# Kernel optimization log

Measured on AMD Instinct MI355X. Metric: run time of the kernel, lower is better.

Reference implementation:

```python
import jax, jax.numpy as jnp
import numpy as np

# FP4 (E2M1) code table: nibble = [sign(1) | exp(2) | mantissa(1)]
# magnitudes for codes 0..7: 0, 0.5, 1, 1.5, 2, 3, 4, 6; codes 8..15 are negated.
_MAG = np.array([0.0, 0.5, 1.0, 1.5, 2.0, 3.0, 4.0, 6.0], dtype=np.float32)
FP4_LUT = jnp.asarray(np.concatenate([_MAG, -_MAG]))  # [16]

BLOCK = 16  # scale-factor block size along in_features


def setup_inputs() -> dict:
    key = jax.random.key(0)
    k0, k1, k2, k3, k4 = jax.random.split(key, 5)
    M, K, N = 32, 8192, 8192  # tokens, in_features, out_features
    inp = jax.random.normal(k0, (M, K), dtype=jnp.float32)
    qweight = jax.random.randint(k1, (N, K // 2), 0, 256, dtype=jnp.int32)  # packed FP4 pairs
    scales = jax.random.uniform(k2, (N, K // BLOCK), dtype=jnp.float32)      # per-block scales
    amax = jax.random.uniform(k3, (1,), dtype=jnp.float32) + 0.5             # global scale
    bias = jax.random.normal(k4, (N,), dtype=jnp.float32)
    return {"input": inp, "qweight": qweight, "scales": scales, "amax": amax, "bias": bias}


def _dequantize(qweight, scales, amax):
    N = qweight.shape[0]
    low = qweight & 0xF            # first element of each pair
    high = (qweight >> 4) & 0xF    # second element
    nibbles = jnp.stack([low, high], axis=-1).reshape(N, -1)  # [N, K]
    vals = FP4_LUT[nibbles]                                   # [N, K] fp4 values
    # per-block scaling: block of BLOCK contiguous in-features shares one scale
    w = (vals.reshape(N, -1, BLOCK) * scales[..., None]).reshape(N, -1)
    return w * amax[0]


def reference(input, qweight, scales, amax, bias):
    weight = _dequantize(qweight, scales, amax)   # [N, K] full-precision weight
    return input @ weight.T + bias                # F.linear
```

## Files before the change

kernel.cpp:

```cpp
#include <hip/hip_runtime.h>
#include <hip/hip_bf16.h>

#define M_DIM 32
#define K_DIM 8192
#define N_DIM 8192
#define KS 8
#define KCH (K_DIM / KS)
#define NGROUPS (N_DIM / 32)
#define TOTAL_WAVES (NGROUPS * KS)
#define MAIN_BLOCKS (TOTAL_WAVES / 4)

typedef _Float16 half8 __attribute__((ext_vector_type(8)));
typedef float floatx4 __attribute__((ext_vector_type(4)));

__device__ __forceinline__ uint32_t dec2(uint32_t q) {
  uint32_t c0 = q & 0xFu, c1 = (q >> 4) & 0xFu;
  uint32_t m0 = c0 & 7u, m1 = c1 & 7u;
  uint32_t t0 = (m0 >= 2u) ? (m0 + 28u) : (m0 ? 28u : 0u);
  uint32_t t1 = (m1 >= 2u) ? (m1 + 28u) : (m1 ? 28u : 0u);
  return (t0 << 9) | ((c0 & 8u) << 12)
       | (t1 << 25) | ((c1 & 8u) << 28);
}

__device__ __forceinline__ half8 decode8(int4 q, float scale) {
  union { uint32_t u[4]; half8 h; } w;
  w.u[0] = dec2((uint32_t)q.x);
  w.u[1] = dec2((uint32_t)q.y);
  w.u[2] = dec2((uint32_t)q.z);
  w.u[3] = dec2((uint32_t)q.w);
  _Float16 s = (_Float16)scale;
  half8 sv = {s, s, s, s, s, s, s, s};
  return w.h * sv;
}

__device__ __forceinline__ half8 loadA(const float* __restrict__ inp, int m, int kq) {
  const floatx4* p = reinterpret_cast<const floatx4*>(inp + m * K_DIM + kq);
  floatx4 f0 = p[0];
  floatx4 f1 = p[1];
  half8 a;
  a[0] = (_Float16)f0[0]; a[1] = (_Float16)f0[1];
  a[2] = (_Float16)f0[2]; a[3] = (_Float16)f0[3];
  a[4] = (_Float16)f1[0]; a[5] = (_Float16)f1[1];
  a[6] = (_Float16)f1[2]; a[7] = (_Float16)f1[3];
  return a;
}

__global__ void init_out_kernel(float* __restrict__ out, const float* __restrict__ bias) {
  int idx = blockIdx.x * blockDim.x + threadIdx.x;
  if (idx < M_DIM * N_DIM) out[idx] = bias[idx & (N_DIM - 1)];
}

__global__ __launch_bounds__(256, 2) void fp4_linear_kernel(
    const float* __restrict__ inp,
    const int4*  __restrict__ qw4,
    const float* __restrict__ scales,
    const float* __restrict__ amaxp,
    float* __restrict__ out)
{
  const int lane = threadIdx.x & 63;
  const int wave = blockIdx.x * 4 + (threadIdx.x >> 6);
  const int ng   = wave & (NGROUPS - 1);
  const int ks   = wave >> 8;
  const int n0   = ng * 32;
  const int kb   = ks * KCH;

  const int row  = lane & 15;
  const int quad = lane >> 4;

  const float amax = amaxp[0];

  floatx4 acc00 = {0.f, 0.f, 0.f, 0.f};
  floatx4 acc01 = {0.f, 0.f, 0.f, 0.f};
  floatx4 acc10 = {0.f, 0.f, 0.f, 0.f};
  floatx4 acc11 = {0.f, 0.f, 0.f, 0.f};

  const int nA = n0 + row;
  const int nB = n0 + 16 + row;
  const int4*  qrowA = qw4 + (size_t)nA * (K_DIM / 8);
  const int4*  qrowB = qw4 + (size_t)nB * (K_DIM / 8);
  const float* srowA = scales + (size_t)nA * (K_DIM / 16);
  const float* srowB = scales + (size_t)nB * (K_DIM / 16);

  for (int k0 = kb; k0 < kb + KCH; k0 += 32) {
    const int kq = k0 + quad * 8;
    int4  qA = qrowA[kq >> 3];
    int4  qB = qrowB[kq >> 3];
    float sA = srowA[kq >> 4] * amax;
    float sB = srowB[kq >> 4] * amax;
    half8 bA = decode8(qA, sA);
    half8 bB = decode8(qB, sB);
    half8 a0 = loadA(inp, row, kq);
    half8 a1 = loadA(inp, row + 16, kq);

    acc00 = __builtin_amdgcn_mfma_f32_16x16x32_f16(a0, bA, acc00, 0, 0, 0);
    acc01 = __builtin_amdgcn_mfma_f32_16x16x32_f16(a0, bB, acc01, 0, 0, 0);
    acc10 = __builtin_amdgcn_mfma_f32_16x16x32_f16(a1, bA, acc10, 0, 0, 0);
    acc11 = __builtin_amdgcn_mfma_f32_16x16x32_f16(a1, bB, acc11, 0, 0, 0);
  }

#pragma unroll
  for (int r = 0; r < 4; ++r) {
    const int m = quad * 4 + r;
    unsafeAtomicAdd(&out[(size_t)m * N_DIM + n0 + row],            acc00[r]);
    unsafeAtomicAdd(&out[(size_t)m * N_DIM + n0 + 16 + row],       acc01[r]);
    unsafeAtomicAdd(&out[(size_t)(m + 16) * N_DIM + n0 + row],      acc10[r]);
    unsafeAtomicAdd(&out[(size_t)(m + 16) * N_DIM + n0 + 16 + row], acc11[r]);
  }
}

extern "C" void kernel_launch(void* const* d_in, const int* in_sizes, int n_in,
                              void* d_out, int out_size, void* d_ws, size_t ws_size,
                              hipStream_t stream) {
  const float* inp    = (const float*)d_in[0];
  const int4*  qw4    = (const int4*)d_in[1];
  const float* scales = (const float*)d_in[2];
  const float* amaxp  = (const float*)d_in[3];
  const float* bias   = (const float*)d_in[4];
  float* out = (float*)d_out;

  init_out_kernel<<<(M_DIM * N_DIM + 255) / 256, 256, 0, stream>>>(out, bias);
  fp4_linear_kernel<<<MAIN_BLOCKS, 256, 0, stream>>>(inp, qw4, scales, amaxp, out);
}
```

Before: 262.2 us.

## Prefetch loads, use hardware FP4 convert, pre-convert input, LDS-reduce split-K partials

Several ideas land together. The K split doubles to 16, and the four waves of a block now work on the same N group so their partial sums are added in shared memory before one atomic per output. Loads are software-pipelined one iteration ahead, and FP4 decode uses the gfx950 scaled convert builtin when it is available. The fp32 input is converted once to fp16 in the workspace, and the bias init is vectorised. These target load latency, decode ALU work, redundant activation conversion and atomic traffic, at the cost of an extra kernel launch and more shared memory per block.

```diff
diff --git a/kernel.cpp b/kernel.cpp
--- a/kernel.cpp
+++ b/kernel.cpp
@@ -4,63 +4,99 @@
 #define M_DIM 32
 #define K_DIM 8192
 #define N_DIM 8192
-#define KS 8
+#define KS 16
 #define KCH (K_DIM / KS)
+#define ITERS (KCH / 32)
 #define NGROUPS (N_DIM / 32)
-#define TOTAL_WAVES (NGROUPS * KS)
-#define MAIN_BLOCKS (TOTAL_WAVES / 4)
+#define MAIN_BLOCKS (NGROUPS * KS / 4)
 
-typedef _Float16 half8 __attribute__((ext_vector_type(8)));
-typedef float floatx4 __attribute__((ext_vector_type(4)));
+typedef _Float16 half8   __attribute__((ext_vector_type(8)));
+typedef _Float16 half4_t __attribute__((ext_vector_type(4)));
+typedef _Float16 half2_t __attribute__((ext_vector_type(2)));
+typedef float    floatx4 __attribute__((ext_vector_type(4)));
 
+#if defined(__has_builtin)
+#if __has_builtin(__builtin_amdgcn_cvt_scalef32_pk_f16_fp4)
+#define HAVE_CVT_FP4 1
+#endif
+#endif
+
+#ifndef HAVE_CVT_FP4
 __device__ __forceinline__ uint32_t dec2(uint32_t q) {
   uint32_t c0 = q & 0xFu, c1 = (q >> 4) & 0xFu;
   uint32_t m0 = c0 & 7u, m1 = c1 & 7u;
-  uint32_t t0 = (m0 >= 2u) ? (m0 + 28u) : (m0 ? 28u : 0u);
-  uint32_t t1 = (m1 >= 2u) ? (m1 + 28u) : (m1 ? 28u : 0u);
+  uint32_t t0 = min(28u * m0, m0 + 28u);
+  uint32_t t1 = min(28u * m1, m1 + 28u);
   return (t0 << 9) | ((c0 & 8u) << 12)
        | (t1 << 25) | ((c1 & 8u) << 28);
 }
+#endif
 
 __device__ __forceinline__ half8 decode8(int4 q, float scale) {
-  union { uint32_t u[4]; half8 h; } w;
+  union { uint32_t u[4]; half2_t h2[4]; half8 h; } w;
+#ifdef HAVE_CVT_FP4
+  w.h2[0] = __builtin_amdgcn_cvt_scalef32_pk_f16_fp4((unsigned)q.x, 1.0f, 0);
+  w.h2[1] = __builtin_amdgcn_cvt_scalef32_pk_f16_fp4((unsigned)q.y, 1.0f, 0);
+  w.h2[2] = __builtin_amdgcn_cvt_scalef32_pk_f16_fp4((unsigned)q.z, 1.0f, 0);
+  w.h2[3] = __builtin_amdgcn_cvt_scalef32_pk_f16_fp4((unsigned)q.w, 1.0f, 0);
+#else
   w.u[0] = dec2((uint32_t)q.x);
   w.u[1] = dec2((uint32_t)q.y);
   w.u[2] = dec2((uint32_t)q.z);
   w.u[3] = dec2((uint32_t)q.w);
+#endif
   _Float16 s = (_Float16)scale;
   half8 sv = {s, s, s, s, s, s, s, s};
   return w.h * sv;
 }
 
-__device__ __forceinline__ half8 loadA(const float* __restrict__ inp, int m, int kq) {
-  const floatx4* p = reinterpret_cast<const floatx4*>(inp + m * K_DIM + kq);
-  floatx4 f0 = p[0];
-  floatx4 f1 = p[1];
-  half8 a;
-  a[0] = (_Float16)f0[0]; a[1] = (_Float16)f0[1];
-  a[2] = (_Float16)f0[2]; a[3] = (_Float16)f0[3];
-  a[4] = (_Float16)f1[0]; a[5] = (_Float16)f1[1];
-  a[6] = (_Float16)f1[2]; a[7] = (_Float16)f1[3];
-  return a;
+template <bool F16A>
+__device__ __forceinline__ half8 loadA(const void* __restrict__ A, int m, int kq) {
+  if constexpr (F16A) {
+    return *reinterpret_cast<const half8*>(
+        (const _Float16*)A + (size_t)m * K_DIM + kq);
+  } else {
+    const floatx4* p =
+        reinterpret_cast<const floatx4*>((const float*)A + (size_t)m * K_DIM + kq);
+    floatx4 f0 = p[0];
+    floatx4 f1 = p[1];
+    half8 a;
+    a[0] = (_Float16)f0[0]; a[1] = (_Float16)f0[1];
+    a[2] = (_Float16)f0[2]; a[3] = (_Float16)f0[3];
+    a[4] = (_Float16)f1[0]; a[5] = (_Float16)f1[1];
+    a[6] = (_Float16)f1[2]; a[7] = (_Float16)f1[3];
+    return a;
+  }
 }
 
-__global__ void init_out_kernel(float* __restrict__ out, const float* __restrict__ bias) {
+__global__ void init_out_kernel(floatx4* __restrict__ out4,
+                                const floatx4* __restrict__ bias4) {
   int idx = blockIdx.x * blockDim.x + threadIdx.x;
-  if (idx < M_DIM * N_DIM) out[idx] = bias[idx & (N_DIM - 1)];
+  out4[idx] = bias4[idx & (N_DIM / 4 - 1)];
 }
 
-__global__ __launch_bounds__(256, 2) void fp4_linear_kernel(
-    const float* __restrict__ inp,
-    const int4*  __restrict__ qw4,
+__global__ void convertA_kernel(const floatx4* __restrict__ in4,
+                                half4_t* __restrict__ out4) {
+  int idx = blockIdx.x * blockDim.x + threadIdx.x;
+  floatx4 f = in4[idx];
+  half4_t h;
+  h[0] = (_Float16)f[0]; h[1] = (_Float16)f[1];
+  h[2] = (_Float16)f[2]; h[3] = (_Float16)f[3];
+  out4[idx] = h;
+}
+
+template <bool F16A>
+__global__ __launch_bounds__(256, 4) void fp4_linear_kernel(
+    const void* __restrict__ Av,
+    const int4* __restrict__ qw4,
     const float* __restrict__ scales,
     const float* __restrict__ amaxp,
     float* __restrict__ out)
 {
   const int lane = threadIdx.x & 63;
-  const int wave = blockIdx.x * 4 + (threadIdx.x >> 6);
-  const int ng   = wave & (NGROUPS - 1);
-  const int ks   = wave >> 8;
+  const int w    = threadIdx.x >> 6;
+  const int ng   = blockIdx.x >> 2;
+  const int ks   = (blockIdx.x & 3) * 4 + w;
   const int n0   = ng * 32;
   const int kb   = ks * KCH;
 
@@ -81,30 +117,56 @@
   const float* srowA = scales + (size_t)nA * (K_DIM / 16);
   const float* srowB = scales + (size_t)nB * (K_DIM / 16);
 
-  for (int k0 = kb; k0 < kb + KCH; k0 += 32) {
-    const int kq = k0 + quad * 8;
-    int4  qA = qrowA[kq >> 3];
-    int4  qB = qrowB[kq >> 3];
-    float sA = srowA[kq >> 4] * amax;
-    float sB = srowB[kq >> 4] * amax;
-    half8 bA = decode8(qA, sA);
-    half8 bB = decode8(qB, sB);
-    half8 a0 = loadA(inp, row, kq);
-    half8 a1 = loadA(inp, row + 16, kq);
+  int kq = kb + quad * 8;
+  int4  qA = qrowA[kq >> 3];
+  int4  qB = qrowB[kq >> 3];
+  float sA = srowA[kq >> 4];
+  float sB = srowB[kq >> 4];
+  half8 a0 = loadA<F16A>(Av, row, kq);
+  half8 a1 = loadA<F16A>(Av, row + 16, kq);
 
+#pragma unroll 4
+  for (int it = 0; it < ITERS; ++it) {
+    const int kqn  = kq + 32;
+    const int qidx = min(kqn >> 3, K_DIM / 8 - 1);
+    const int sidx = min(kqn >> 4, K_DIM / 16 - 1);
+    const int aidx = min(kqn, K_DIM - 8);
+    int4  qA_n = qrowA[qidx];
+    int4  qB_n = qrowB[qidx];
+    float sA_n = srowA[sidx];
+    float sB_n = srowB[sidx];
+    half8 a0_n = loadA<F16A>(Av, row, aidx);
+    half8 a1_n = loadA<F16A>(Av, row + 16, aidx);
+
+    half8 bA = decode8(qA, sA * amax);
+    half8 bB = decode8(qB, sB * amax);
     acc00 = __builtin_amdgcn_mfma_f32_16x16x32_f16(a0, bA, acc00, 0, 0, 0);
     acc01 = __builtin_amdgcn_mfma_f32_16x16x32_f16(a0, bB, acc01, 0, 0, 0);
     acc10 = __builtin_amdgcn_mfma_f32_16x16x32_f16(a1, bA, acc10, 0, 0, 0);
     acc11 = __builtin_amdgcn_mfma_f32_16x16x32_f16(a1, bB, acc11, 0, 0, 0);
+
+    qA = qA_n; qB = qB_n; sA = sA_n; sB = sB_n; a0 = a0_n; a1 = a1_n;
+    kq = kqn;
   }
 
+  __shared__ float red[4 * 32 * 34];
+  float* slab = red + w * (32 * 34);
 #pragma unroll
   for (int r = 0; r < 4; ++r) {
     const int m = quad * 4 + r;
-    unsafeAtomicAdd(&out[(size_t)m * N_DIM + n0 + row],            acc00[r]);
-    unsafeAtomicAdd(&out[(size_t)m * N_DIM + n0 + 16 + row],       acc01[r]);
-    unsafeAtomicAdd(&out[(size_t)(m + 16) * N_DIM + n0 + row],      acc10[r]);
-    unsafeAtomicAdd(&out[(size_t)(m + 16) * N_DIM + n0 + 16 + row], acc11[r]);
+    slab[m * 34 + row]             = acc00[r];
+    slab[m * 34 + 16 + row]        = acc01[r];
+    slab[(m + 16) * 34 + row]      = acc10[r];
+    slab[(m + 16) * 34 + 16 + row] = acc11[r];
+  }
+  __syncthreads();
+#pragma unroll
+  for (int i = 0; i < 4; ++i) {
+    const int o = i * 256 + threadIdx.x;
+    const int m = o >> 5, n = o & 31;
+    const int a = m * 34 + n;
+    float v = red[a] + red[1088 + a] + red[2 * 1088 + a] + red[3 * 1088 + a];
+    unsafeAtomicAdd(&out[(size_t)m * N_DIM + n0 + n], v);
   }
 }
 
@@ -118,6 +180,17 @@
   const float* bias   = (const float*)d_in[4];
   float* out = (float*)d_out;
 
-  init_out_kernel<<<(M_DIM * N_DIM + 255) / 256, 256, 0, stream>>>(out, bias);
-  fp4_linear_kernel<<<MAIN_BLOCKS, 256, 0, stream>>>(inp, qw4, scales, amaxp, out);
+  init_out_kernel<<<M_DIM * N_DIM / 4 / 256, 256, 0, stream>>>(
+      (floatx4*)out, (const floatx4*)bias);
+
+  const bool f16a = ws_size >= (size_t)M_DIM * K_DIM * sizeof(_Float16);
+  if (f16a) {
+    convertA_kernel<<<M_DIM * K_DIM / 4 / 256, 256, 0, stream>>>(
+        (const floatx4*)inp, (half4_t*)d_ws);
+    fp4_linear_kernel<true><<<MAIN_BLOCKS, 256, 0, stream>>>(
+        d_ws, qw4, scales, amaxp, out);
+  } else {
+    fp4_linear_kernel<false><<<MAIN_BLOCKS, 256, 0, stream>>>(
+        inp, qw4, scales, amaxp, out);
+  }
 }
```

Measured after the change: 236.7 us. 1.11x faster.

## Stage activations and scales in LDS, prefetch weights, use hardware FP4 convert

Applied to the files above, without the earlier changes.

Each block now converts its K-slice of the fp32 activations to fp16 once and stores it in shared memory, along with the prescaled block scales, so the four waves that share it stop reloading from global memory. The K split goes from 8 to 32 and the occupancy hint from 2 to 6, the weight loads are software-prefetched one iteration ahead, and the FP4 decode uses the hardware cvt_scalef32_pk_f16_fp4 builtin when the compiler provides it. The bias init is vectorised to float4. In exchange there are more atomic adds into the output (32-way K split), a higher LDS footprint, and a barrier after the staging phase.

```diff
diff --git a/kernel.cpp b/kernel.cpp
--- a/kernel.cpp
+++ b/kernel.cpp
@@ -4,107 +4,163 @@
 #define M_DIM 32
 #define K_DIM 8192
 #define N_DIM 8192
-#define KS 8
+#define KS 32
 #define KCH (K_DIM / KS)
-#define NGROUPS (N_DIM / 32)
-#define TOTAL_WAVES (NGROUPS * KS)
-#define MAIN_BLOCKS (TOTAL_WAVES / 4)
+#define ITERS (KCH / 32)
+#define NGPB 4
+#define MAIN_BLOCKS ((N_DIM / 32 / NGPB) * KS)
 
-typedef _Float16 half8 __attribute__((ext_vector_type(8)));
-typedef float floatx4 __attribute__((ext_vector_type(4)));
+#define A_STRIDE (KCH + 8)
+#define S_STRIDE (KCH / 16 + 1)
 
+typedef _Float16 half8   __attribute__((ext_vector_type(8)));
+typedef _Float16 half2_t __attribute__((ext_vector_type(2)));
+typedef float    floatx4 __attribute__((ext_vector_type(4)));
+
+#if defined(__has_builtin)
+#if __has_builtin(__builtin_amdgcn_cvt_scalef32_pk_f16_fp4)
+#define HAVE_CVT_FP4 1
+#endif
+#endif
+
+#ifndef HAVE_CVT_FP4
 __device__ __forceinline__ uint32_t dec2(uint32_t q) {
   uint32_t c0 = q & 0xFu, c1 = (q >> 4) & 0xFu;
   uint32_t m0 = c0 & 7u, m1 = c1 & 7u;
-  uint32_t t0 = (m0 >= 2u) ? (m0 + 28u) : (m0 ? 28u : 0u);
-  uint32_t t1 = (m1 >= 2u) ? (m1 + 28u) : (m1 ? 28u : 0u);
+  uint32_t t0 = min(28u * m0, m0 + 28u);
+  uint32_t t1 = min(28u * m1, m1 + 28u);
   return (t0 << 9) | ((c0 & 8u) << 12)
        | (t1 << 25) | ((c1 & 8u) << 28);
 }
+#endif
 
 __device__ __forceinline__ half8 decode8(int4 q, float scale) {
-  union { uint32_t u[4]; half8 h; } w;
+  union { uint32_t u[4]; half2_t h2[4]; half8 h; } w;
+#ifdef HAVE_CVT_FP4
+  w.h2[0] = __builtin_amdgcn_cvt_scalef32_pk_f16_fp4((unsigned)q.x, 1.0f, 0);
+  w.h2[1] = __builtin_amdgcn_cvt_scalef32_pk_f16_fp4((unsigned)q.y, 1.0f, 0);
+  w.h2[2] = __builtin_amdgcn_cvt_scalef32_pk_f16_fp4((unsigned)q.z, 1.0f, 0);
+  w.h2[3] = __builtin_amdgcn_cvt_scalef32_pk_f16_fp4((unsigned)q.w, 1.0f, 0);
+#else
   w.u[0] = dec2((uint32_t)q.x);
   w.u[1] = dec2((uint32_t)q.y);
   w.u[2] = dec2((uint32_t)q.z);
   w.u[3] = dec2((uint32_t)q.w);
+#endif
   _Float16 s = (_Float16)scale;
   half8 sv = {s, s, s, s, s, s, s, s};
   return w.h * sv;
 }
 
-__device__ __forceinline__ half8 loadA(const float* __restrict__ inp, int m, int kq) {
-  const floatx4* p = reinterpret_cast<const floatx4*>(inp + m * K_DIM + kq);
-  floatx4 f0 = p[0];
-  floatx4 f1 = p[1];
-  half8 a;
-  a[0] = (_Float16)f0[0]; a[1] = (_Float16)f0[1];
-  a[2] = (_Float16)f0[2]; a[3] = (_Float16)f0[3];
-  a[4] = (_Float16)f1[0]; a[5] = (_Float16)f1[1];
-  a[6] = (_Float16)f1[2]; a[7] = (_Float16)f1[3];
-  return a;
+__global__ void init_out_kernel(floatx4* __restrict__ out4,
+                                const floatx4* __restrict__ bias4) {
+  int idx = blockIdx.x * blockDim.x + threadIdx.x;
+  out4[idx] = bias4[idx & (N_DIM / 4 - 1)];
 }
 
-__global__ void init_out_kernel(float* __restrict__ out, const float* __restrict__ bias) {
-  int idx = blockIdx.x * blockDim.x + threadIdx.x;
-  if (idx < M_DIM * N_DIM) out[idx] = bias[idx & (N_DIM - 1)];
-}
-
-__global__ __launch_bounds__(256, 2) void fp4_linear_kernel(
+__global__ __launch_bounds__(256, 6) void fp4_linear_kernel(
     const float* __restrict__ inp,
     const int4*  __restrict__ qw4,
     const float* __restrict__ scales,
     const float* __restrict__ amaxp,
     float* __restrict__ out)
 {
-  const int lane = threadIdx.x & 63;
-  const int wave = blockIdx.x * 4 + (threadIdx.x >> 6);
-  const int ng   = wave & (NGROUPS - 1);
-  const int ks   = wave >> 8;
-  const int n0   = ng * 32;
+  __shared__ _Float16 As[M_DIM * A_STRIDE];
+  __shared__ float    Ss[NGPB * 32 * S_STRIDE];
+
+  const int t    = threadIdx.x;
+  const int lane = t & 63;
+  const int w    = t >> 6;
+  const int ks   = blockIdx.x & (KS - 1);
+  const int gb   = blockIdx.x >> 5;
+  const int n0   = gb * (NGPB * 32);
   const int kb   = ks * KCH;
+
+  const float amax = amaxp[0];
+
+  {
+    const float* src = inp + kb;
+    for (int p = 0; p < 4; ++p) {
+      const int idx = p * 256 + t;
+      const int m = idx >> 5, c = idx & 31;
+      const floatx4* g =
+          reinterpret_cast<const floatx4*>(src + (size_t)m * K_DIM + c * 8);
+      floatx4 f0 = g[0], f1 = g[1];
+      half8 h;
+      h[0] = (_Float16)f0[0]; h[1] = (_Float16)f0[1];
+      h[2] = (_Float16)f0[2]; h[3] = (_Float16)f0[3];
+      h[4] = (_Float16)f1[0]; h[5] = (_Float16)f1[1];
+      h[6] = (_Float16)f1[2]; h[7] = (_Float16)f1[3];
+      *reinterpret_cast<half8*>(&As[m * A_STRIDE + c * 8]) = h;
+    }
+  }
+  {
+    const int r = t >> 1, part = t & 1;
+    const float* g = scales + (size_t)(n0 + r) * (K_DIM / 16)
+                   + ks * (KCH / 16) + part * 8;
+    floatx4 f0 = ((const floatx4*)g)[0];
+    floatx4 f1 = ((const floatx4*)g)[1];
+    float* d = &Ss[r * S_STRIDE + part * 8];
+    d[0] = f0[0] * amax; d[1] = f0[1] * amax;
+    d[2] = f0[2] * amax; d[3] = f0[3] * amax;
+    d[4] = f1[0] * amax; d[5] = f1[1] * amax;
+    d[6] = f1[2] * amax; d[7] = f1[3] * amax;
+  }
+  __syncthreads();
 
   const int row  = lane & 15;
   const int quad = lane >> 4;
+  const int nloc = w * 32;
 
-  const float amax = amaxp[0];
+  const int nA = n0 + nloc + row;
+  const int nB = nA + 16;
+  const int4* qrowA = qw4 + (size_t)nA * (K_DIM / 8);
+  const int4* qrowB = qw4 + (size_t)nB * (K_DIM / 8);
+  const _Float16* arow0 = &As[row * A_STRIDE];
+  const _Float16* arow1 = &As[(row + 16) * A_STRIDE];
+  const float* sAp = &Ss[(nloc + row) * S_STRIDE];
+  const float* sBp = &Ss[(nloc + 16 + row) * S_STRIDE];
 
   floatx4 acc00 = {0.f, 0.f, 0.f, 0.f};
   floatx4 acc01 = {0.f, 0.f, 0.f, 0.f};
   floatx4 acc10 = {0.f, 0.f, 0.f, 0.f};
   floatx4 acc11 = {0.f, 0.f, 0.f, 0.f};
 
-  const int nA = n0 + row;
-  const int nB = n0 + 16 + row;
-  const int4*  qrowA = qw4 + (size_t)nA * (K_DIM / 8);
-  const int4*  qrowB = qw4 + (size_t)nB * (K_DIM / 8);
-  const float* srowA = scales + (size_t)nA * (K_DIM / 16);
-  const float* srowB = scales + (size_t)nB * (K_DIM / 16);
+  int kq = kb + quad * 8;
+  int4 qA = qrowA[kq >> 3];
+  int4 qB = qrowB[kq >> 3];
 
-  for (int k0 = kb; k0 < kb + KCH; k0 += 32) {
-    const int kq = k0 + quad * 8;
-    int4  qA = qrowA[kq >> 3];
-    int4  qB = qrowB[kq >> 3];
-    float sA = srowA[kq >> 4] * amax;
-    float sB = srowB[kq >> 4] * amax;
-    half8 bA = decode8(qA, sA);
-    half8 bB = decode8(qB, sB);
-    half8 a0 = loadA(inp, row, kq);
-    half8 a1 = loadA(inp, row + 16, kq);
+#pragma unroll
+  for (int it = 0; it < ITERS; ++it) {
+    const int nidx = min((kq + 32) >> 3, K_DIM / 8 - 1);
+    int4 qA_n = qrowA[nidx];
+    int4 qB_n = qrowB[nidx];
+
+    const int klo = it * 32 + quad * 8;
+    half8 a0 = *reinterpret_cast<const half8*>(arow0 + klo);
+    half8 a1 = *reinterpret_cast<const half8*>(arow1 + klo);
+    const int kbl = klo >> 4;
+    half8 bA = decode8(qA, sAp[kbl]);
+    half8 bB = decode8(qB, sBp[kbl]);
 
     acc00 = __builtin_amdgcn_mfma_f32_16x16x32_f16(a0, bA, acc00, 0, 0, 0);
     acc01 = __builtin_amdgcn_mfma_f32_16x16x32_f16(a0, bB, acc01, 0, 0, 0);
     acc10 = __builtin_amdgcn_mfma_f32_16x16x32_f16(a1, bA, acc10, 0, 0, 0);
     acc11 = __builtin_amdgcn_mfma_f32_16x16x32_f16(a1, bB, acc11, 0, 0, 0);
+
+    qA = qA_n; qB = qB_n;
+    kq += 32;
   }
 
 #pragma unroll
   for (int r = 0; r < 4; ++r) {
     const int m = quad * 4 + r;
-    unsafeAtomicAdd(&out[(size_t)m * N_DIM + n0 + row],            acc00[r]);
-    unsafeAtomicAdd(&out[(size_t)m * N_DIM + n0 + 16 + row],       acc01[r]);
-    unsafeAtomicAdd(&out[(size_t)(m + 16) * N_DIM + n0 + row],      acc10[r]);
-    unsafeAtomicAdd(&out[(size_t)(m + 16) * N_DIM + n0 + 16 + row], acc11[r]);
+    float* o0 = out + (size_t)m * N_DIM + n0 + nloc;
+    float* o1 = out + (size_t)(m + 16) * N_DIM + n0 + nloc;
+    unsafeAtomicAdd(o0 + row,      acc00[r]);
+    unsafeAtomicAdd(o0 + 16 + row, acc01[r]);
+    unsafeAtomicAdd(o1 + row,      acc10[r]);
+    unsafeAtomicAdd(o1 + 16 + row, acc11[r]);
   }
 }
 
@@ -118,6 +174,8 @@
   const float* bias   = (const float*)d_in[4];
   float* out = (float*)d_out;
 
-  init_out_kernel<<<(M_DIM * N_DIM + 255) / 256, 256, 0, stream>>>(out, bias);
-  fp4_linear_kernel<<<MAIN_BLOCKS, 256, 0, stream>>>(inp, qw4, scales, amaxp, out);
+  init_out_kernel<<<M_DIM * N_DIM / 4 / 256, 256, 0, stream>>>(
+      (floatx4*)out, (const floatx4*)bias);
+  fp4_linear_kernel<<<MAIN_BLOCKS, 256, 0, stream>>>(
+      inp, qw4, scales, amaxp, out);
 }
```

Result: faster. 236.3 us (-9.9%).
